# Kernel optimization log

Measured on AMD Instinct MI355X. Metric: run time of the kernel, lower is better.

The kernel has to match this reference:

```python
import jax, jax.numpy as jnp
import numpy as np

T, N, E = 8, 20000, 320000
F_IN, HID, HEADS, GH = 32, 64, 4, 128


def setup_inputs() -> dict:
    key = jax.random.key(0)
    ks = jax.random.split(key, 20)
    rn = lambda k, s, sc=0.05: jax.random.normal(k, s, jnp.float32) * sc
    return {
        "x_seq": jax.random.normal(ks[0], (T, N, F_IN), jnp.float32),
        "edge_index": jax.random.randint(ks[1], (2, E), 0, N),
        # GATConv 1: in=F_IN, out=HID, heads=HEADS, concat=True
        "W1": rn(ks[2], (F_IN, HEADS * HID)),
        "a_src1": rn(ks[3], (HEADS, HID)),
        "a_dst1": rn(ks[4], (HEADS, HID)),
        "b1": jnp.zeros((HEADS * HID,), jnp.float32),
        # GATConv 2: in=HEADS*HID, out=HID, heads=1, concat=False
        "W2": rn(ks[5], (HEADS * HID, HID)),
        "a_src2": rn(ks[6], (1, HID)),
        "a_dst2": rn(ks[7], (1, HID)),
        "b2": jnp.zeros((HID,), jnp.float32),
        # GRU layer 0 (input 2*HID) and layer 1 (input GH); torch gate order r,z,n
        "Wih0": rn(ks[8], (3 * GH, 2 * HID)),
        "Whh0": rn(ks[9], (3 * GH, GH)),
        "bih0": jnp.zeros((3 * GH,), jnp.float32),
        "bhh0": jnp.zeros((3 * GH,), jnp.float32),
        "Wih1": rn(ks[10], (3 * GH, GH)),
        "Whh1": rn(ks[11], (3 * GH, GH)),
        "bih1": jnp.zeros((3 * GH,), jnp.float32),
        "bhh1": jnp.zeros((3 * GH,), jnp.float32),
        # decoder MLP
        "Wd1": rn(ks[12], (GH, GH // 2)),
        "bd1": jnp.zeros((GH // 2,), jnp.float32),
        "Wd2": rn(ks[13], (GH // 2, 1)),
        "bd2": jnp.zeros((1,), jnp.float32),
    }


def _gat(x, W, a_s, a_d, b, src, dst, heads, out_ch, concat):
    """PyG-style GATConv with self-loops already included in (src, dst)."""
    n = x.shape[0]
    h = (x @ W).reshape(n, heads, out_ch)            # [N, H, C]
    al_s = (h * a_s).sum(-1)                          # [N, H]
    al_d = (h * a_d).sum(-1)
    e = jax.nn.leaky_relu(al_s[src] + al_d[dst], 0.2)  # [Etot, H]
    m = jax.ops.segment_max(e, dst, num_segments=n)
    ex = jnp.exp(e - m[dst])
    s = jax.ops.segment_sum(ex, dst, num_segments=n)
    att = ex / (s[dst] + 1e-16)
    out = jax.ops.segment_sum(h[src] * att[..., None], dst, num_segments=n)
    out = out.reshape(n, heads * out_ch) if concat else out.mean(axis=1)
    return out + b


def _gru_layer(xs, Wih, Whh, bih, bhh):
    # xs: [T, B, D]; torch GRU cell, gate order r,z,n
    def step(hp, x):
        gi = x @ Wih.T + bih
        gh = hp @ Whh.T + bhh
        ir, iz, inn = jnp.split(gi, 3, axis=-1)
        hr, hz, hn = jnp.split(gh, 3, axis=-1)
        r = jax.nn.sigmoid(ir + hr)
        z = jax.nn.sigmoid(iz + hz)
        nn_ = jnp.tanh(inn + r * hn)
        h = (1.0 - z) * nn_ + z * hp
        return h, h
    h0 = jnp.zeros((xs.shape[1], Whh.shape[1]), xs.dtype)
    hT, ys = jax.lax.scan(step, h0, xs)
    return hT, ys


def reference(x_seq, edge_index, W1, a_src1, a_dst1, b1, W2, a_src2, a_dst2, b2,
              Wih0, Whh0, bih0, bhh0, Wih1, Whh1, bih1, bhh1, Wd1, bd1, Wd2, bd2):
    n = x_seq.shape[1]
    loops = jnp.arange(n)
    src = jnp.concatenate([edge_index[0], loops])
    dst = jnp.concatenate([edge_index[1], loops])

    def encode(x):                                    # x: [N, F_IN]
        h = jax.nn.elu(_gat(x, W1, a_src1, a_dst1, b1, src, dst, HEADS, HID, True))
        h = _gat(h, W2, a_src2, a_dst2, b2, src, dst, 1, HID, False)
        return jnp.concatenate([h[edge_index[0]], h[edge_index[1]]], axis=-1)  # [E, 2*HID]

    emb = jax.vmap(encode)(x_seq)                     # [T, E, 2*HID]
    _, ys0 = _gru_layer(emb, Wih0, Whh0, bih0, bhh0)
    hT1, _ = _gru_layer(ys0, Wih1, Whh1, bih1, bhh1)  # last-layer final hidden [E, GH]
    pred = jax.nn.relu(hT1 @ Wd1 + bd1) @ Wd2 + bd2   # [E, 1]
    return pred
```

## Files before the change

### kernel.cpp

```cpp
#include <hip/hip_runtime.h>
#include <hip/hip_fp16.h>
#include <math.h>

#define T_ 8
#define N_ 20000
#define E_ 320000
#define ETOT_ (E_ + N_)
#define FIN_ 32
#define C1_ 256
#define HID_ 64
#define G3_ 384
#define GH_ 128
#define MB_ 64
#define MT_ 4
#define LDP_ 136
#define NPACK_ (24 * 4 * 64 * 8)

typedef __attribute__((ext_vector_type(8))) _Float16 h8v;
typedef __attribute__((ext_vector_type(4))) float f4v;

__device__ __forceinline__ float wave_sum(float v) {
#pragma unroll
  for (int off = 32; off; off >>= 1) v += __shfl_down(v, off);
  return v;
}
__device__ __forceinline__ float sigmoidf_(float x) { return 1.f / (1.f + __expf(-x)); }
__device__ __forceinline__ float tanhf_(float x) {
  float e2 = __expf(2.f * x);
  return 1.f - 2.f / (e2 + 1.f);
}
__device__ __forceinline__ unsigned short f2h(float f) {
  return __half_as_ushort(__float2half_rn(f));
}
__device__ __forceinline__ float h2f(unsigned short u) {
  return __half2float(__ushort_as_half(u));
}
__device__ __forceinline__ void edge_sd(const int* ei, int e, int& s, int& d) {
  if (e < E_) { s = ei[e]; d = ei[E_ + e]; }
  else { s = e - E_; d = e - E_; }
}

__global__ void k_hist(const int* __restrict__ ei, int* __restrict__ counts) {
  int e = blockIdx.x * 256 + threadIdx.x;
  if (e >= ETOT_) return;
  int s, d; edge_sd(ei, e, s, d);
  atomicAdd(&counts[d], 1);
}

__global__ void k_scan(const int* __restrict__ counts, int* __restrict__ indptr) {
  __shared__ int tmp[1024];
  __shared__ int carry;
  int tid = threadIdx.x;
  if (tid == 0) { carry = 0; indptr[0] = 0; }
  __syncthreads();
  for (int base = 0; base < N_; base += 1024) {
    int i = base + tid;
    int v = (i < N_) ? counts[i] : 0;
    tmp[tid] = v;
    __syncthreads();
    for (int off = 1; off < 1024; off <<= 1) {
      int add = (tid >= off) ? tmp[tid - off] : 0;
      __syncthreads();
      tmp[tid] += add;
      __syncthreads();
    }
    if (i < N_) indptr[i + 1] = carry + tmp[tid];
    __syncthreads();
    if (tid == 1023) carry += tmp[1023];
    __syncthreads();
  }
}

__global__ void k_copy(const int* __restrict__ indptr, int* __restrict__ cursors) {
  int i = blockIdx.x * 256 + threadIdx.x;
  if (i < N_) cursors[i] = indptr[i];
}

__global__ void k_scatter(const int* __restrict__ ei, int* __restrict__ cursors,
                          int* __restrict__ csr_src) {
  int e = blockIdx.x * 256 + threadIdx.x;
  if (e >= ETOT_) return;
  int s, d; edge_sd(ei, e, s, d);
  int pos = atomicAdd(&cursors[d], 1);
  csr_src[pos] = s;
}

__global__ void k_packW16(const float* __restrict__ W, unsigned short* __restrict__ Bh) {
  int idx = blockIdx.x * 256 + threadIdx.x;
  if (idx >= NPACK_) return;
  int j = idx & 7, lane = (idx >> 3) & 63, ks = (idx >> 9) & 3, nt = idx >> 11;
  int n = nt * 16 + (lane & 15);
  int k = ks * 32 + (lane >> 4) * 8 + j;
  Bh[idx] = f2h(W[n * GH_ + k]);
}

__global__ __launch_bounds__(256) void k_gat1_lin(
    const float* __restrict__ x, size_t xs, const float* __restrict__ W1,
    const float* __restrict__ as1, const float* __restrict__ ad1,
    unsigned short* __restrict__ hlin, size_t hs,
    float* __restrict__ als, float* __restrict__ ald, size_t avs) {
  size_t t = blockIdx.y;
  x += t * xs; hlin += t * hs; als += t * avs; ald += t * avs;
  int n = blockIdx.x;
  int j = threadIdx.x;
  __shared__ float sx[FIN_];
  if (j < FIN_) sx[j] = x[n * FIN_ + j];
  __syncthreads();
  float acc = 0.f;
#pragma unroll
  for (int k = 0; k < FIN_; ++k) acc = fmaf(sx[k], W1[k * C1_ + j], acc);
  hlin[(size_t)n * C1_ + j] = f2h(acc);
  int h = j >> 6, c = j & 63;
  float vs = wave_sum(acc * as1[h * 64 + c]);
  float vd = wave_sum(acc * ad1[h * 64 + c]);
  if (c == 0) { als[n * 4 + h] = vs; ald[n * 4 + h] = vd; }
}

__global__ __launch_bounds__(256) void k_gat1_attn(
    const int* __restrict__ csr_src, const int* __restrict__ indptr,
    const float* __restrict__ als, const float* __restrict__ ald, size_t avs,
    float* __restrict__ ex, size_t exs, float* __restrict__ sums, size_t ss) {
  size_t t = blockIdx.y;
  als += t * avs; ald += t * avs; ex += t * exs; sums += t * ss;
  int w = threadIdx.x >> 6, lane = threadIdx.x & 63;
  int n = blockIdx.x * 4 + w;
  int s0 = indptr[n], s1 = indptr[n + 1];
  float adv[4], mx[4], sm[4];
#pragma unroll
  for (int h = 0; h < 4; ++h) { adv[h] = ald[n * 4 + h]; mx[h] = -1e30f; sm[h] = 0.f; }
  for (int e = s0 + lane; e < s1; e += 64) {
    int s = csr_src[e];
#pragma unroll
    for (int h = 0; h < 4; ++h) {
      float sc = als[s * 4 + h] + adv[h];
      sc = sc >= 0.f ? sc : 0.2f * sc;
      ex[(size_t)e * 4 + h] = sc;
      mx[h] = fmaxf(mx[h], sc);
    }
  }
#pragma unroll
  for (int h = 0; h < 4; ++h) {
#pragma unroll
    for (int off = 32; off; off >>= 1) mx[h] = fmaxf(mx[h], __shfl_xor(mx[h], off));
  }
  for (int e = s0 + lane; e < s1; e += 64) {
#pragma unroll
    for (int h = 0; h < 4; ++h) {
      float v = __expf(ex[(size_t)e * 4 + h] - mx[h]);
      ex[(size_t)e * 4 + h] = v;
      sm[h] += v;
    }
  }
#pragma unroll
  for (int h = 0; h < 4; ++h) sm[h] = wave_sum(sm[h]);
  if (lane == 0) {
#pragma unroll
    for (int h = 0; h < 4; ++h) sums[n * 4 + h] = sm[h];
  }
}

__global__ __launch_bounds__(256) void k_agg1lin2(
    const int* __restrict__ csr_src, const int* __restrict__ indptr,
    const float* __restrict__ ex, size_t exs, const float* __restrict__ sums, size_t ss,
    const unsigned short* __restrict__ hlin, size_t hs, const float* __restrict__ b1,
    const float* __restrict__ W2, const float* __restrict__ as2, const float* __restrict__ ad2,
    unsigned short* __restrict__ hlin2, size_t h2s,
    float* __restrict__ als2, float* __restrict__ ald2, size_t a2s) {
  size_t t = blockIdx.y;
  ex += t * exs; sums += t * ss; hlin += t * hs;
  hlin2 += t * h2s; als2 += t * a2s; ald2 += t * a2s;
  int n = blockIdx.x;
  int j = threadIdx.x;
  int w = j >> 6, lane = j & 63;
  __shared__ float sh1[C1_];
  __shared__ float part[4][68];
  int s0 = indptr[n], s1 = indptr[n + 1];
  float inv = 1.f / (sums[n * 4 + w] + 1e-16f);
  float acc = 0.f;
  int e = s0;
  for (; e + 4 <= s1; e += 4) {
    int i0 = csr_src[e], i1 = csr_src[e + 1], i2 = csr_src[e + 2], i3 = csr_src[e + 3];
    float a0 = ex[(size_t)(e + 0) * 4 + w] * inv;
    float a1 = ex[(size_t)(e + 1) * 4 + w] * inv;
    float a2 = ex[(size_t)(e + 2) * 4 + w] * inv;
    float a3 = ex[(size_t)(e + 3) * 4 + w] * inv;
    float g0 = h2f(hlin[(size_t)i0 * C1_ + j]);
    float g1 = h2f(hlin[(size_t)i1 * C1_ + j]);
    float g2 = h2f(hlin[(size_t)i2 * C1_ + j]);
    float g3 = h2f(hlin[(size_t)i3 * C1_ + j]);
    acc = fmaf(a0, g0, acc);
    acc = fmaf(a1, g1, acc);
    acc = fmaf(a2, g2, acc);
    acc = fmaf(a3, g3, acc);
  }
  for (; e < s1; ++e) {
    int s = csr_src[e];
    acc = fmaf(ex[(size_t)e * 4 + w] * inv, h2f(hlin[(size_t)s * C1_ + j]), acc);
  }
  float o = acc + b1[j];
  sh1[j] = o > 0.f ? o : expm1f(o);
  __syncthreads();
  float pw = 0.f;
#pragma unroll 4
  for (int kk = 0; kk < 64; ++kk) {
    int k = w * 64 + kk;
    pw = fmaf(sh1[k], W2[k * HID_ + lane], pw);
  }
  part[w][lane] = pw;
  __syncthreads();
  if (w == 0) {
    float a2 = part[0][lane] + part[1][lane] + part[2][lane] + part[3][lane];
    hlin2[(size_t)n * HID_ + lane] = f2h(a2);
    float vs = wave_sum(a2 * as2[lane]);
    float vd = wave_sum(a2 * ad2[lane]);
    if (lane == 0) { als2[n] = vs; ald2[n] = vd; }
  }
}

__global__ __launch_bounds__(256) void k_gat2_attn(
    const int* __restrict__ csr_src, const int* __restrict__ indptr,
    const float* __restrict__ als, const float* __restrict__ ald, size_t a2s,
    float* __restrict__ ex, size_t e2s, float* __restrict__ sums, size_t s2s) {
  size_t t = blockIdx.y;
  als += t * a2s; ald += t * a2s; ex += t * e2s; sums += t * s2s;
  int w = threadIdx.x >> 6, lane = threadIdx.x & 63;
  int n = blockIdx.x * 4 + w;
  int s0 = indptr[n], s1 = indptr[n + 1];
  float adv = ald[n];
  float mx = -1e30f, sm = 0.f;
  for (int e = s0 + lane; e < s1; e += 64) {
    float sc = als[csr_src[e]] + adv;
    sc = sc >= 0.f ? sc : 0.2f * sc;
    ex[e] = sc;
    mx = fmaxf(mx, sc);
  }
#pragma unroll
  for (int off = 32; off; off >>= 1) mx = fmaxf(mx, __shfl_xor(mx, off));
  for (int e = s0 + lane; e < s1; e += 64) {
    float v = __expf(ex[e] - mx);
    ex[e] = v;
    sm += v;
  }
  sm = wave_sum(sm);
  if (lane == 0) sums[n] = sm;
}

__global__ __launch_bounds__(256) void k_gat2_agg(
    const int* __restrict__ csr_src, const int* __restrict__ indptr,
    const float* __restrict__ ex, size_t e2s, const float* __restrict__ sums, size_t s2s,
    const unsigned short* __restrict__ hlin2, size_t h2s, const float* __restrict__ b2,
    unsigned short* __restrict__ h2f16, size_t hos) {
  size_t t = blockIdx.y;
  ex += t * e2s; sums += t * s2s; hlin2 += t * h2s; h2f16 += t * hos;
  int w = threadIdx.x >> 6, lane = threadIdx.x & 63;
  int n = blockIdx.x * 4 + w;
  int s0 = indptr[n], s1 = indptr[n + 1];
  float inv = 1.f / (sums[n] + 1e-16f);
  float acc = 0.f;
  int e = s0;
  for (; e + 4 <= s1; e += 4) {
    int i0 = csr_src[e], i1 = csr_src[e + 1], i2 = csr_src[e + 2], i3 = csr_src[e + 3];
    float a0 = ex[e + 0] * inv;
    float a1 = ex[e + 1] * inv;
    float a2 = ex[e + 2] * inv;
    float a3 = ex[e + 3] * inv;
    float g0 = h2f(hlin2[(size_t)i0 * HID_ + lane]);
    float g1 = h2f(hlin2[(size_t)i1 * HID_ + lane]);
    float g2 = h2f(hlin2[(size_t)i2 * HID_ + lane]);
    float g3 = h2f(hlin2[(size_t)i3 * HID_ + lane]);
    acc = fmaf(a0, g0, acc);
    acc = fmaf(a1, g1, acc);
    acc = fmaf(a2, g2, acc);
    acc = fmaf(a3, g3, acc);
  }
  for (; e < s1; ++e) {
    int s = csr_src[e];
    acc = fmaf(ex[e] * inv, h2f(hlin2[(size_t)s * HID_ + lane]), acc);
  }
  h2f16[(size_t)n * HID_ + lane] = f2h(acc + b2[lane]);
}

__device__ __forceinline__ void mfma1h(f4v& acc, h8v a, h8v b) {
  acc = __builtin_amdgcn_mfma_f32_16x16x32_f16(a, b, acc, 0, 0, 0);
}

__device__ __forceinline__ void mfma_pass(
    const unsigned short* A_,
    const unsigned short* __restrict__ Bh_,
    int w, int lane, f4v Cr[MT_], f4v Cz[MT_], f4v Cn[MT_]) {
  const int mrow = lane & 15, quad = lane >> 4;
#pragma unroll
  for (int ks = 0; ks < 4; ++ks) {
    h8v A[MT_];
    const int aoff = mrow * LDP_ + ks * 32 + quad * 8;
#pragma unroll
    for (int mt = 0; mt < MT_; ++mt) A[mt] = *(const h8v*)(A_ + aoff + mt * (16 * LDP_));
    {
      const int nt = w;
      const h8v bh = *(const h8v*)(Bh_ + ((size_t)(nt * 4 + ks) * 64 + lane) * 8);
#pragma unroll
      for (int mt = 0; mt < MT_; ++mt) mfma1h(Cr[mt], A[mt], bh);
    }
    {
      const int nt = 8 + w;
      const h8v bh = *(const h8v*)(Bh_ + ((size_t)(nt * 4 + ks) * 64 + lane) * 8);
#pragma unroll
      for (int mt = 0; mt < MT_; ++mt) mfma1h(Cz[mt], A[mt], bh);
    }
    {
      const int nt = 16 + w;
      const h8v bh = *(const h8v*)(Bh_ + ((size_t)(nt * 4 + ks) * 64 + lane) * 8);
#pragma unroll
      for (int mt = 0; mt < MT_; ++mt) mfma1h(Cn[mt], A[mt], bh);
    }
  }
}

__device__ __forceinline__ void mfma_pass_x(
    const unsigned short* __restrict__ h2,
    const int esrc[MT_], const int edst[MT_],
    const unsigned short* __restrict__ Bh_,
    int w, int lane, f4v Cr[MT_], f4v Cz[MT_], f4v Cn[MT_]) {
  const int quad = lane >> 4;
#pragma unroll
  for (int ks = 0; ks < 4; ++ks) {
    h8v A[MT_];
    const int choff = (ks & 1) * 32 + quad * 8;
#pragma unroll
    for (int mt = 0; mt < MT_; ++mt) {
      const int node = (ks < 2) ? esrc[mt] : edst[mt];
      A[mt] = *(const h8v*)(h2 + (size_t)node * HID_ + choff);
    }
    {
      const int nt = w;
      const h8v bh = *(const h8v*)(Bh_ + ((size_t)(nt * 4 + ks) * 64 + lane) * 8);
#pragma unroll
      for (int mt = 0; mt < MT_; ++mt) mfma1h(Cr[mt], A[mt], bh);
    }
    {
      const int nt = 8 + w;
      const h8v bh = *(const h8v*)(Bh_ + ((size_t)(nt * 4 + ks) * 64 + lane) * 8);
#pragma unroll
      for (int mt = 0; mt < MT_; ++mt) mfma1h(Cz[mt], A[mt], bh);
    }
    {
      const int nt = 16 + w;
      const h8v bh = *(const h8v*)(Bh_ + ((size_t)(nt * 4 + ks) * 64 + lane) * 8);
#pragma unroll
      for (int mt = 0; mt < MT_; ++mt) mfma1h(Cn[mt], A[mt], bh);
    }
  }
}

__global__ __launch_bounds__(512, 4) void k_gru_step(
    const unsigned short* __restrict__ h2, const int* __restrict__ ei,
    int seg_e0, int first, int last,
    const unsigned short* __restrict__ pWih0, const unsigned short* __restrict__ pWhh0,
    const unsigned short* __restrict__ pWih1, const unsigned short* __restrict__ pWhh1,
    const float* __restrict__ bih0, const float* __restrict__ bhh0,
    const float* __restrict__ bih1, const float* __restrict__ bhh1,
    const float* __restrict__ Wd1, const float* __restrict__ bd1,
    const float* __restrict__ Wd2, const float* __restrict__ bd2,
    unsigned short* __restrict__ h0g, unsigned short* __restrict__ h1g,
    float* __restrict__ out) {
  __shared__ unsigned short h0h[MB_ * LDP_];
  __shared__ unsigned short h1h[MB_ * LDP_];
  const int tid = threadIdx.x;
  const int lane = tid & 63, w = tid >> 6;
  const int col = lane & 15, quad = lane >> 4;
  const int mrow = lane & 15;
  const int le0 = blockIdx.x * MB_;
  const size_t ge0 = (size_t)seg_e0 + le0;

  if (!first) {
    for (int i = tid; i < MB_ * 16; i += 512) {
      int e = i >> 4, c = (i & 15) * 8;
      *(h8v*)&h0h[e * LDP_ + c] =
          __builtin_nontemporal_load((const h8v*)(h0g + (size_t)(le0 + e) * GH_ + c));
      *(h8v*)&h1h[e * LDP_ + c] =
          __builtin_nontemporal_load((const h8v*)(h1g + (size_t)(le0 + e) * GH_ + c));
    }
  }
  int esrc[MT_], edst[MT_];
#pragma unroll
  for (int mt = 0; mt < MT_; ++mt) {
    esrc[mt] = ei[ge0 + mt * 16 + mrow];
    edst[mt] = ei[E_ + ge0 + mt * 16 + mrow];
  }
  __syncthreads();

  const int cg = w * 16 + col;
  f4v Cr[MT_], Cz[MT_], Cin[MT_], Chn[MT_];

#pragma unroll
  for (int mt = 0; mt < MT_; ++mt) {
    Cr[mt] = (f4v){0.f, 0.f, 0.f, 0.f};
    Cz[mt] = (f4v){0.f, 0.f, 0.f, 0.f};
    Cin[mt] = (f4v){0.f, 0.f, 0.f, 0.f};
    Chn[mt] = (f4v){0.f, 0.f, 0.f, 0.f};
  }
  mfma_pass_x(h2, esrc, edst, pWih0, w, lane, Cr, Cz, Cin);
  if (!first) mfma_pass(h0h, pWhh0, w, lane, Cr, Cz, Chn);
  __syncthreads();
  {
    float biR = bih0[cg] + bhh0[cg];
    float biZ = bih0[128 + cg] + bhh0[128 + cg];
    float biNi = bih0[256 + cg], biNh = bhh0[256 + cg];
#pragma unroll
    for (int mt = 0; mt < MT_; ++mt)
#pragma unroll
      for (int reg = 0; reg < 4; ++reg) {
        int e = mt * 16 + quad * 4 + reg;
        float r = sigmoidf_(Cr[mt][reg] + biR);
        float z = sigmoidf_(Cz[mt][reg] + biZ);
        float n = tanhf_(Cin[mt][reg] + biNi + r * (Chn[mt][reg] + biNh));
        float hp = first ? 0.f : h2f(h0h[e * LDP_ + cg]);
        float hv = (1.f - z) * n + z * hp;
        h0h[e * LDP_ + cg] = f2h(hv);
      }
  }
  __syncthreads();

#pragma unroll
  for (int mt = 0; mt < MT_; ++mt) {
    Cr[mt] = (f4v){0.f, 0.f, 0.f, 0.f};
    Cz[mt] = (f4v){0.f, 0.f, 0.f, 0.f};
    Cin[mt] = (f4v){0.f, 0.f, 0.f, 0.f};
    Chn[mt] = (f4v){0.f, 0.f, 0.f, 0.f};
  }
  mfma_pass(h0h, pWih1, w, lane, Cr, Cz, Cin);
  if (!first) mfma_pass(h1h, pWhh1, w, lane, Cr, Cz, Chn);
  __syncthreads();
  {
    float biR = bih1[cg] + bhh1[cg];
    float biZ = bih1[128 + cg] + bhh1[128 + cg];
    float biNi = bih1[256 + cg], biNh = bhh1[256 + cg];
#pragma unroll
    for (int mt = 0; mt < MT_; ++mt)
#pragma unroll
      for (int reg = 0; reg < 4; ++reg) {
        int e = mt * 16 + quad * 4 + reg;
        float r = sigmoidf_(Cr[mt][reg] + biR);
        float z = sigmoidf_(Cz[mt][reg] + biZ);
        float n = tanhf_(Cin[mt][reg] + biNi + r * (Chn[mt][reg] + biNh));
        float hp = first ? 0.f : h2f(h1h[e * LDP_ + cg]);
        float hv = (1.f - z) * n + z * hp;
        if (!last) {
          h1h[e * LDP_ + cg] = f2h(hv);
        } else {
          unsigned short hb = f2h(hv);
          h1h[e * LDP_ + cg] = hb;
          h0h[e * LDP_ + cg] = f2h(hv - h2f(hb));
        }
      }
  }
  __syncthreads();

  if (!last) {
    for (int i = tid; i < MB_ * 16; i += 512) {
      int e = i >> 4, c = (i & 15) * 8;
      __builtin_nontemporal_store(*(const h8v*)&h0h[e * LDP_ + c],
                                  (h8v*)(h0g + (size_t)(le0 + e) * GH_ + c));
      __builtin_nontemporal_store(*(const h8v*)&h1h[e * LDP_ + c],
                                  (h8v*)(h1g + (size_t)(le0 + e) * GH_ + c));
    }
  } else {
    for (int ee = 0; ee < MB_ / 8; ++ee) {
      int e = w * (MB_ / 8) + ee;
      float acc = 0.f;
#pragma unroll
      for (int kc = 0; kc < 16; ++kc) {
        h8v hv8 = *(const h8v*)&h1h[e * LDP_ + kc * 8];
        h8v lv8 = *(const h8v*)&h0h[e * LDP_ + kc * 8];
#pragma unroll
        for (int j = 0; j < 8; ++j) {
          float hvv = (float)hv8[j] + (float)lv8[j];
          acc = fmaf(hvv, Wd1[(kc * 8 + j) * 64 + lane], acc);
        }
      }
      float rv = fmaxf(acc + bd1[lane], 0.f);
      float contrib = wave_sum(rv * Wd2[lane]);
      if (lane == 0) out[ge0 + e] = contrib + bd2[0];
    }
  }
}

extern "C" void kernel_launch(void* const* d_in, const int* in_sizes, int n_in,
                              void* d_out, int out_size, void* d_ws, size_t ws_size,
                              hipStream_t stream) {
  (void)in_sizes; (void)n_in; (void)out_size;
  const float* x_seq = (const float*)d_in[0];
  const int*   ei    = (const int*)d_in[1];
  const float* W1    = (const float*)d_in[2];
  const float* as1   = (const float*)d_in[3];
  const float* ad1   = (const float*)d_in[4];
  const float* b1    = (const float*)d_in[5];
  const float* W2    = (const float*)d_in[6];
  const float* as2   = (const float*)d_in[7];
  const float* ad2   = (const float*)d_in[8];
  const float* b2    = (const float*)d_in[9];
  const float* Wih0  = (const float*)d_in[10];
  const float* Whh0  = (const float*)d_in[11];
  const float* bih0  = (const float*)d_in[12];
  const float* bhh0  = (const float*)d_in[13];
  const float* Wih1  = (const float*)d_in[14];
  const float* Whh1  = (const float*)d_in[15];
  const float* bih1  = (const float*)d_in[16];
  const float* bhh1  = (const float*)d_in[17];
  const float* Wd1   = (const float*)d_in[18];
  const float* bd1   = (const float*)d_in[19];
  const float* Wd2   = (const float*)d_in[20];
  const float* bd2   = (const float*)d_in[21];
  float* out = (float*)d_out;

  char* p = (char*)d_ws;
  auto alloc = [&](size_t bytes) -> char* {
    char* r = p;
    p += (bytes + 255) & ~(size_t)255;
    return r;
  };
  auto rnd = [](size_t b) { return (b + 255) & ~(size_t)255; };

  unsigned short* h2_all = (unsigned short*)alloc((size_t)T_ * N_ * HID_ * 2);
  unsigned short* pWih0 = (unsigned short*)alloc(NPACK_ * 2);
  unsigned short* pWhh0 = (unsigned short*)alloc(NPACK_ * 2);
  unsigned short* pWih1 = (unsigned short*)alloc(NPACK_ * 2);
  unsigned short* pWhh1 = (unsigned short*)alloc(NPACK_ * 2);
  int* counts   = (int*)alloc((size_t)N_ * 4);
  int* indptr   = (int*)alloc((size_t)(N_ + 1) * 4);
  int* cursors  = (int*)alloc((size_t)N_ * 4);
  int* csr      = (int*)alloc((size_t)ETOT_ * 4);

  const size_t S_HL1 = (size_t)N_ * C1_;
  const size_t S_EX1 = (size_t)ETOT_ * 4;
  const size_t S_SU1 = (size_t)N_ * 4;
  const size_t S_HL2 = (size_t)N_ * HID_;
  const size_t S_EX2 = (size_t)ETOT_;
  const size_t S_SC2 = (size_t)N_;

  size_t gat_batched = rnd(S_HL1 * 2 * T_) + rnd(S_EX1 * 4 * T_) + 3 * rnd(S_SU1 * 4 * T_) +
                       rnd(S_HL2 * 2 * T_) + rnd(S_EX2 * 4 * T_) + 3 * rnd(S_SC2 * 4 * T_);
  size_t states1 = 2 * rnd((size_t)E_ * GH_ * 2);
  size_t pers_off = (size_t)(p - (char*)d_ws);
  size_t need_b = gat_batched > states1 ? gat_batched : states1;
  const int batched = (ws_size >= pers_off + need_b + (1u << 20)) ? 1 : 0;
  const size_t TB = batched ? T_ : 1;
  const int segs = batched ? 1 : 2;
  const int eseg = E_ / segs;

  char* region = p;
  unsigned short* hlin1 = (unsigned short*)alloc(S_HL1 * 2 * TB);
  float* ex1    = (float*)alloc(S_EX1 * 4 * TB);
  float* als1   = (float*)alloc(S_SU1 * 4 * TB);
  float* ald1   = (float*)alloc(S_SU1 * 4 * TB);
  float* sums1  = (float*)alloc(S_SU1 * 4 * TB);
  unsigned short* hlin2 = (unsigned short*)alloc(S_HL2 * 2 * TB);
  float* ex2    = (float*)alloc(S_EX2 * 4 * TB);
  float* als2   = (float*)alloc(S_SC2 * 4 * TB);
  float* ald2   = (float*)alloc(S_SC2 * 4 * TB);
  float* sums2  = (float*)alloc(S_SC2 * 4 * TB);
  unsigned short* h0g = (unsigned short*)(region);
  unsigned short* h1g = (unsigned short*)(region + rnd((size_t)eseg * GH_ * 2));

  (void)hipMemsetAsync(counts, 0, (size_t)N_ * 4, stream);

  k_hist<<<(ETOT_ + 255) / 256, 256, 0, stream>>>(ei, counts);
  k_scan<<<1, 1024, 0, stream>>>(counts, indptr);
  k_copy<<<(N_ + 255) / 256, 256, 0, stream>>>(indptr, cursors);
  k_scatter<<<(ETOT_ + 255) / 256, 256, 0, stream>>>(ei, cursors, csr);
  const int pb = (NPACK_ + 255) / 256;
  k_packW16<<<pb, 256, 0, stream>>>(Wih0, pWih0);
  k_packW16<<<pb, 256, 0, stream>>>(Whh0, pWhh0);
  k_packW16<<<pb, 256, 0, stream>>>(Wih1, pWih1);
  k_packW16<<<pb, 256, 0, stream>>>(Whh1, pWhh1);

  const int TL = batched ? 1 : T_;
  const unsigned gy = batched ? T_ : 1;
  for (int t = 0; t < TL; ++t) {
    const float* xt = batched ? x_seq : x_seq + (size_t)t * N_ * FIN_;
    unsigned short* h2t = batched ? h2_all : h2_all + (size_t)t * N_ * HID_;
    k_gat1_lin<<<dim3(N_, gy), 256, 0, stream>>>(
        xt, (size_t)N_ * FIN_, W1, as1, ad1, hlin1, S_HL1, als1, ald1, S_SU1);
    k_gat1_attn<<<dim3(N_ / 4, gy), 256, 0, stream>>>(
        csr, indptr, als1, ald1, S_SU1, ex1, S_EX1, sums1, S_SU1);
    k_agg1lin2<<<dim3(N_, gy), 256, 0, stream>>>(
        csr, indptr, ex1, S_EX1, sums1, S_SU1, hlin1, S_HL1, b1,
        W2, as2, ad2, hlin2, S_HL2, als2, ald2, S_SC2);
    k_gat2_attn<<<dim3(N_ / 4, gy), 256, 0, stream>>>(
        csr, indptr, als2, ald2, S_SC2, ex2, S_EX2, sums2, S_SC2);
    k_gat2_agg<<<dim3(N_ / 4, gy), 256, 0, stream>>>(
        csr, indptr, ex2, S_EX2, sums2, S_SC2, hlin2, S_HL2, b2, h2t, S_HL2);
  }

  for (int seg = 0; seg < segs; ++seg) {
    for (int t = 0; t < T_; ++t) {
      const unsigned short* h2t = h2_all + (size_t)t * N_ * HID_;
      k_gru_step<<<eseg / MB_, 512, 0, stream>>>(
          h2t, ei, seg * eseg, (t == 0) ? 1 : 0, (t == T_ - 1) ? 1 : 0,
          pWih0, pWhh0, pWih1, pWhh1,
          bih0, bhh0, bih1, bhh1, Wd1, bd1, Wd2, bd2,
          h0g, h1g, out);
    }
  }
}
```

Baseline: 4.245 ms.

## Recompute GAT attention scores on the fly instead of storing per-edge buffers

Removes the per-edge ex1/ex2 buffers. The attention kernels now store only the per-node max and sum, and the aggregation kernels recompute leaky_relu and exp from the gathered per-node als values. This trades extra gathers and exp work for eliminating several passes over edge-sized arrays, and it also shrinks workspace so the batched path fits more easily. Separately, the GRU step loads its edge indices earlier and moves a barrier to after the input MFMA pass, so the hidden-state shared-memory load overlaps with that pass.

```diff
diff --git a/kernel.cpp b/kernel.cpp
--- a/kernel.cpp
+++ b/kernel.cpp
@@ -119,9 +119,9 @@
 __global__ __launch_bounds__(256) void k_gat1_attn(
     const int* __restrict__ csr_src, const int* __restrict__ indptr,
     const float* __restrict__ als, const float* __restrict__ ald, size_t avs,
-    float* __restrict__ ex, size_t exs, float* __restrict__ sums, size_t ss) {
+    float* __restrict__ sums, float* __restrict__ mxs, size_t ss) {
   size_t t = blockIdx.y;
-  als += t * avs; ald += t * avs; ex += t * exs; sums += t * ss;
+  als += t * avs; ald += t * avs; sums += t * ss; mxs += t * ss;
   int w = threadIdx.x >> 6, lane = threadIdx.x & 63;
   int n = blockIdx.x * 4 + w;
   int s0 = indptr[n], s1 = indptr[n + 1];
@@ -134,7 +134,6 @@
     for (int h = 0; h < 4; ++h) {
       float sc = als[s * 4 + h] + adv[h];
       sc = sc >= 0.f ? sc : 0.2f * sc;
-      ex[(size_t)e * 4 + h] = sc;
       mx[h] = fmaxf(mx[h], sc);
     }
   }
@@ -144,30 +143,32 @@
     for (int off = 32; off; off >>= 1) mx[h] = fmaxf(mx[h], __shfl_xor(mx[h], off));
   }
   for (int e = s0 + lane; e < s1; e += 64) {
+    int s = csr_src[e];
 #pragma unroll
     for (int h = 0; h < 4; ++h) {
-      float v = __expf(ex[(size_t)e * 4 + h] - mx[h]);
-      ex[(size_t)e * 4 + h] = v;
-      sm[h] += v;
+      float sc = als[s * 4 + h] + adv[h];
+      sc = sc >= 0.f ? sc : 0.2f * sc;
+      sm[h] += __expf(sc - mx[h]);
     }
   }
 #pragma unroll
   for (int h = 0; h < 4; ++h) sm[h] = wave_sum(sm[h]);
   if (lane == 0) {
 #pragma unroll
-    for (int h = 0; h < 4; ++h) sums[n * 4 + h] = sm[h];
+    for (int h = 0; h < 4; ++h) { sums[n * 4 + h] = sm[h]; mxs[n * 4 + h] = mx[h]; }
   }
 }
 
 __global__ __launch_bounds__(256) void k_agg1lin2(
     const int* __restrict__ csr_src, const int* __restrict__ indptr,
-    const float* __restrict__ ex, size_t exs, const float* __restrict__ sums, size_t ss,
+    const float* __restrict__ als, const float* __restrict__ ald,
+    const float* __restrict__ sums, const float* __restrict__ mxs, size_t ss,
     const unsigned short* __restrict__ hlin, size_t hs, const float* __restrict__ b1,
     const float* __restrict__ W2, const float* __restrict__ as2, const float* __restrict__ ad2,
     unsigned short* __restrict__ hlin2, size_t h2s,
     float* __restrict__ als2, float* __restrict__ ald2, size_t a2s) {
   size_t t = blockIdx.y;
-  ex += t * exs; sums += t * ss; hlin += t * hs;
+  als += t * ss; ald += t * ss; sums += t * ss; mxs += t * ss; hlin += t * hs;
   hlin2 += t * h2s; als2 += t * a2s; ald2 += t * a2s;
   int n = blockIdx.x;
   int j = threadIdx.x;
@@ -176,14 +177,24 @@
   __shared__ float part[4][68];
   int s0 = indptr[n], s1 = indptr[n + 1];
   float inv = 1.f / (sums[n * 4 + w] + 1e-16f);
+  float mxw = mxs[n * 4 + w];
+  float adv = ald[n * 4 + w];
   float acc = 0.f;
   int e = s0;
   for (; e + 4 <= s1; e += 4) {
     int i0 = csr_src[e], i1 = csr_src[e + 1], i2 = csr_src[e + 2], i3 = csr_src[e + 3];
-    float a0 = ex[(size_t)(e + 0) * 4 + w] * inv;
-    float a1 = ex[(size_t)(e + 1) * 4 + w] * inv;
-    float a2 = ex[(size_t)(e + 2) * 4 + w] * inv;
-    float a3 = ex[(size_t)(e + 3) * 4 + w] * inv;
+    float s0v = als[i0 * 4 + w] + adv;
+    float s1v = als[i1 * 4 + w] + adv;
+    float s2v = als[i2 * 4 + w] + adv;
+    float s3v = als[i3 * 4 + w] + adv;
+    s0v = s0v >= 0.f ? s0v : 0.2f * s0v;
+    s1v = s1v >= 0.f ? s1v : 0.2f * s1v;
+    s2v = s2v >= 0.f ? s2v : 0.2f * s2v;
+    s3v = s3v >= 0.f ? s3v : 0.2f * s3v;
+    float a0 = __expf(s0v - mxw) * inv;
+    float a1 = __expf(s1v - mxw) * inv;
+    float a2 = __expf(s2v - mxw) * inv;
+    float a3 = __expf(s3v - mxw) * inv;
     float g0 = h2f(hlin[(size_t)i0 * C1_ + j]);
     float g1 = h2f(hlin[(size_t)i1 * C1_ + j]);
     float g2 = h2f(hlin[(size_t)i2 * C1_ + j]);
@@ -195,7 +206,9 @@
   }
   for (; e < s1; ++e) {
     int s = csr_src[e];
-    acc = fmaf(ex[(size_t)e * 4 + w] * inv, h2f(hlin[(size_t)s * C1_ + j]), acc);
+    float sc = als[s * 4 + w] + adv;
+    sc = sc >= 0.f ? sc : 0.2f * sc;
+    acc = fmaf(__expf(sc - mxw) * inv, h2f(hlin[(size_t)s * C1_ + j]), acc);
   }
   float o = acc + b1[j];
   sh1[j] = o > 0.f ? o : expm1f(o);
@@ -220,9 +233,9 @@
 __global__ __launch_bounds__(256) void k_gat2_attn(
     const int* __restrict__ csr_src, const int* __restrict__ indptr,
     const float* __restrict__ als, const float* __restrict__ ald, size_t a2s,
-    float* __restrict__ ex, size_t e2s, float* __restrict__ sums, size_t s2s) {
+    float* __restrict__ sums, float* __restrict__ mxs, size_t s2s) {
   size_t t = blockIdx.y;
-  als += t * a2s; ald += t * a2s; ex += t * e2s; sums += t * s2s;
+  als += t * a2s; ald += t * a2s; sums += t * s2s; mxs += t * s2s;
   int w = threadIdx.x >> 6, lane = threadIdx.x & 63;
   int n = blockIdx.x * 4 + w;
   int s0 = indptr[n], s1 = indptr[n + 1];
@@ -231,39 +244,50 @@
   for (int e = s0 + lane; e < s1; e += 64) {
     float sc = als[csr_src[e]] + adv;
     sc = sc >= 0.f ? sc : 0.2f * sc;
-    ex[e] = sc;
     mx = fmaxf(mx, sc);
   }
 #pragma unroll
   for (int off = 32; off; off >>= 1) mx = fmaxf(mx, __shfl_xor(mx, off));
   for (int e = s0 + lane; e < s1; e += 64) {
-    float v = __expf(ex[e] - mx);
-    ex[e] = v;
-    sm += v;
+    float sc = als[csr_src[e]] + adv;
+    sc = sc >= 0.f ? sc : 0.2f * sc;
+    sm += __expf(sc - mx);
   }
   sm = wave_sum(sm);
-  if (lane == 0) sums[n] = sm;
+  if (lane == 0) { sums[n] = sm; mxs[n] = mx; }
 }
 
 __global__ __launch_bounds__(256) void k_gat2_agg(
     const int* __restrict__ csr_src, const int* __restrict__ indptr,
-    const float* __restrict__ ex, size_t e2s, const float* __restrict__ sums, size_t s2s,
+    const float* __restrict__ als, const float* __restrict__ ald,
+    const float* __restrict__ sums, const float* __restrict__ mxs, size_t s2s,
     const unsigned short* __restrict__ hlin2, size_t h2s, const float* __restrict__ b2,
     unsigned short* __restrict__ h2f16, size_t hos) {
   size_t t = blockIdx.y;
-  ex += t * e2s; sums += t * s2s; hlin2 += t * h2s; h2f16 += t * hos;
+  als += t * s2s; ald += t * s2s; sums += t * s2s; mxs += t * s2s;
+  hlin2 += t * h2s; h2f16 += t * hos;
   int w = threadIdx.x >> 6, lane = threadIdx.x & 63;
   int n = blockIdx.x * 4 + w;
   int s0 = indptr[n], s1 = indptr[n + 1];
   float inv = 1.f / (sums[n] + 1e-16f);
+  float mxv = mxs[n];
+  float adv = ald[n];
   float acc = 0.f;
   int e = s0;
   for (; e + 4 <= s1; e += 4) {
     int i0 = csr_src[e], i1 = csr_src[e + 1], i2 = csr_src[e + 2], i3 = csr_src[e + 3];
-    float a0 = ex[e + 0] * inv;
-    float a1 = ex[e + 1] * inv;
-    float a2 = ex[e + 2] * inv;
-    float a3 = ex[e + 3] * inv;
+    float s0v = als[i0] + adv;
+    float s1v = als[i1] + adv;
+    float s2v = als[i2] + adv;
+    float s3v = als[i3] + adv;
+    s0v = s0v >= 0.f ? s0v : 0.2f * s0v;
+    s1v = s1v >= 0.f ? s1v : 0.2f * s1v;
+    s2v = s2v >= 0.f ? s2v : 0.2f * s2v;
+    s3v = s3v >= 0.f ? s3v : 0.2f * s3v;
+    float a0 = __expf(s0v - mxv) * inv;
+    float a1 = __expf(s1v - mxv) * inv;
+    float a2 = __expf(s2v - mxv) * inv;
+    float a3 = __expf(s3v - mxv) * inv;
     float g0 = h2f(hlin2[(size_t)i0 * HID_ + lane]);
     float g1 = h2f(hlin2[(size_t)i1 * HID_ + lane]);
     float g2 = h2f(hlin2[(size_t)i2 * HID_ + lane]);
@@ -275,7 +299,9 @@
   }
   for (; e < s1; ++e) {
     int s = csr_src[e];
-    acc = fmaf(ex[e] * inv, h2f(hlin2[(size_t)s * HID_ + lane]), acc);
+    float sc = als[s] + adv;
+    sc = sc >= 0.f ? sc : 0.2f * sc;
+    acc = fmaf(__expf(sc - mxv) * inv, h2f(hlin2[(size_t)s * HID_ + lane]), acc);
   }
   h2f16[(size_t)n * HID_ + lane] = f2h(acc + b2[lane]);
 }
@@ -372,6 +398,12 @@
   const int le0 = blockIdx.x * MB_;
   const size_t ge0 = (size_t)seg_e0 + le0;
 
+  int esrc[MT_], edst[MT_];
+#pragma unroll
+  for (int mt = 0; mt < MT_; ++mt) {
+    esrc[mt] = ei[ge0 + mt * 16 + mrow];
+    edst[mt] = ei[E_ + ge0 + mt * 16 + mrow];
+  }
   if (!first) {
     for (int i = tid; i < MB_ * 16; i += 512) {
       int e = i >> 4, c = (i & 15) * 8;
@@ -381,13 +413,6 @@
           __builtin_nontemporal_load((const h8v*)(h1g + (size_t)(le0 + e) * GH_ + c));
     }
   }
-  int esrc[MT_], edst[MT_];
-#pragma unroll
-  for (int mt = 0; mt < MT_; ++mt) {
-    esrc[mt] = ei[ge0 + mt * 16 + mrow];
-    edst[mt] = ei[E_ + ge0 + mt * 16 + mrow];
-  }
-  __syncthreads();
 
   const int cg = w * 16 + col;
   f4v Cr[MT_], Cz[MT_], Cin[MT_], Chn[MT_];
@@ -400,6 +425,7 @@
     Chn[mt] = (f4v){0.f, 0.f, 0.f, 0.f};
   }
   mfma_pass_x(h2, esrc, edst, pWih0, w, lane, Cr, Cz, Cin);
+  __syncthreads();
   if (!first) mfma_pass(h0h, pWhh0, w, lane, Cr, Cz, Chn);
   __syncthreads();
   {
@@ -532,14 +558,12 @@
   int* csr      = (int*)alloc((size_t)ETOT_ * 4);
 
   const size_t S_HL1 = (size_t)N_ * C1_;
-  const size_t S_EX1 = (size_t)ETOT_ * 4;
   const size_t S_SU1 = (size_t)N_ * 4;
   const size_t S_HL2 = (size_t)N_ * HID_;
-  const size_t S_EX2 = (size_t)ETOT_;
   const size_t S_SC2 = (size_t)N_;
 
-  size_t gat_batched = rnd(S_HL1 * 2 * T_) + rnd(S_EX1 * 4 * T_) + 3 * rnd(S_SU1 * 4 * T_) +
-                       rnd(S_HL2 * 2 * T_) + rnd(S_EX2 * 4 * T_) + 3 * rnd(S_SC2 * 4 * T_);
+  size_t gat_batched = rnd(S_HL1 * 2 * T_) + 4 * rnd(S_SU1 * 4 * T_) +
+                       rnd(S_HL2 * 2 * T_) + 4 * rnd(S_SC2 * 4 * T_);
   size_t states1 = 2 * rnd((size_t)E_ * GH_ * 2);
   size_t pers_off = (size_t)(p - (char*)d_ws);
   size_t need_b = gat_batched > states1 ? gat_batched : states1;
@@ -550,15 +574,15 @@
 
   char* region = p;
   unsigned short* hlin1 = (unsigned short*)alloc(S_HL1 * 2 * TB);
-  float* ex1    = (float*)alloc(S_EX1 * 4 * TB);
   float* als1   = (float*)alloc(S_SU1 * 4 * TB);
   float* ald1   = (float*)alloc(S_SU1 * 4 * TB);
   float* sums1  = (float*)alloc(S_SU1 * 4 * TB);
+  float* mxs1   = (float*)alloc(S_SU1 * 4 * TB);
   unsigned short* hlin2 = (unsigned short*)alloc(S_HL2 * 2 * TB);
-  float* ex2    = (float*)alloc(S_EX2 * 4 * TB);
   float* als2   = (float*)alloc(S_SC2 * 4 * TB);
   float* ald2   = (float*)alloc(S_SC2 * 4 * TB);
   float* sums2  = (float*)alloc(S_SC2 * 4 * TB);
+  float* mxs2   = (float*)alloc(S_SC2 * 4 * TB);
   unsigned short* h0g = (unsigned short*)(region);
   unsigned short* h1g = (unsigned short*)(region + rnd((size_t)eseg * GH_ * 2));
 
@@ -582,14 +606,14 @@
     k_gat1_lin<<<dim3(N_, gy), 256, 0, stream>>>(
         xt, (size_t)N_ * FIN_, W1, as1, ad1, hlin1, S_HL1, als1, ald1, S_SU1);
     k_gat1_attn<<<dim3(N_ / 4, gy), 256, 0, stream>>>(
-        csr, indptr, als1, ald1, S_SU1, ex1, S_EX1, sums1, S_SU1);
+        csr, indptr, als1, ald1, S_SU1, sums1, mxs1, S_SU1);
     k_agg1lin2<<<dim3(N_, gy), 256, 0, stream>>>(
-        csr, indptr, ex1, S_EX1, sums1, S_SU1, hlin1, S_HL1, b1,
+        csr, indptr, als1, ald1, sums1, mxs1, S_SU1, hlin1, S_HL1, b1,
         W2, as2, ad2, hlin2, S_HL2, als2, ald2, S_SC2);
     k_gat2_attn<<<dim3(N_ / 4, gy), 256, 0, stream>>>(
-        csr, indptr, als2, ald2, S_SC2, ex2, S_EX2, sums2, S_SC2);
+        csr, indptr, als2, ald2, S_SC2, sums2, mxs2, S_SC2);
     k_gat2_agg<<<dim3(N_ / 4, gy), 256, 0, stream>>>(
-        csr, indptr, ex2, S_EX2, sums2, S_SC2, hlin2, S_HL2, b2, h2t, S_HL2);
+        csr, indptr, als2, ald2, sums2, mxs2, S_SC2, hlin2, S_HL2, b2, h2t, S_HL2);
   }
 
   for (int seg = 0; seg < segs; ++seg) {
```

Result: no change. 4.201 ms, median of 2 (-1.0%).
